# Kernel optimization log

Hardware: AMD Instinct MI355X
Metric: run time of the kernel (lower is better)

Reference implementation:

```python
import jax, jax.numpy as jnp
import numpy as np

TOP_K = 2


def setup_inputs() -> dict:
    key = jax.random.key(0)
    ks = jax.random.split(key, 5)
    B, N, C, FF, E = 2, 2048, 1024, 4096, 8
    x = jax.random.normal(ks[0], (B, N, C), dtype=jnp.float32)
    router_w = jax.random.normal(ks[1], (E, C), dtype=jnp.float32) * 0.02
    # xavier-uniform-like init for expert weights
    lim1 = np.sqrt(6.0 / (FF + C))
    expert_w1 = jax.random.uniform(ks[2], (E, FF, C), dtype=jnp.float32, minval=-lim1, maxval=lim1)
    expert_b1 = jnp.zeros((E, FF), dtype=jnp.float32)
    expert_w2 = jax.random.uniform(ks[3], (E, C, FF), dtype=jnp.float32, minval=-lim1, maxval=lim1)
    expert_b2 = jnp.zeros((E, C), dtype=jnp.float32)
    return {"x": x, "router_w": router_w, "expert_w1": expert_w1,
            "expert_b1": expert_b1, "expert_w2": expert_w2, "expert_b2": expert_b2}


def reference(x, router_w, expert_w1, expert_b1, expert_w2, expert_b2):
    # x: [B,N,C]; router_w: [E,C]; expert_w1: [E,FF,C]; expert_w2: [E,C,FF]
    router_logits = jnp.einsum('bnc,ec->bne', x, router_w)          # [B,N,E]
    router_probs = jax.nn.softmax(router_logits, axis=-1)
    expert_weights, expert_idx = jax.lax.top_k(router_probs, TOP_K)  # [B,N,K]
    expert_weights = expert_weights / (expert_weights.sum(axis=-1, keepdims=True) + 1e-9)
    # Dense all-expert FFN (avoids materializing per-token gathered weight matrices)
    h = jnp.einsum('bnc,efc->bnef', x, expert_w1) + expert_b1        # [B,N,E,FF]
    h = jax.nn.gelu(h, approximate=False)                            # torch nn.GELU = exact
    out_all = jnp.einsum('bnef,ecf->bnec', h, expert_w2) + expert_b2  # [B,N,E,C]
    # Gather top-k expert outputs and combine
    out_k = jnp.take_along_axis(out_all, expert_idx[..., None], axis=2)  # [B,N,K,C]
    return (out_k * expert_weights[..., None]).sum(axis=2)           # [B,N,C]
```

## Files before the change

kernel.cpp:

```cpp
#include <hip/hip_runtime.h>
#include <hip/hip_bf16.h>
#include <cstdint>

#define TTOK  4096
#define CDIM  1024
#define FFDIM 4096
#define NEXP  8


typedef short short8 __attribute__((ext_vector_type(8)));
typedef float f32x4 __attribute__((ext_vector_type(4)));

__device__ __forceinline__ unsigned short f2bf(float f) {
    unsigned int u = __float_as_uint(f);
    u = u + 0x7fffu + ((u >> 16) & 1u);
    return (unsigned short)(u >> 16);
}

__device__ __forceinline__ void gl_lds16(const unsigned short* g, unsigned short* l) {
    __builtin_amdgcn_global_load_lds(
        (const __attribute__((address_space(1))) unsigned int*)g,
        (__attribute__((address_space(3))) unsigned int*)l, 16, 0, 0);
}

__global__ void cast_kernel(const float* __restrict__ src, unsigned short* __restrict__ dst) {
    int i = blockIdx.x * blockDim.x + threadIdx.x;
    float4 v = reinterpret_cast<const float4*>(src)[i];
    ushort4 o;
    o.x = f2bf(v.x); o.y = f2bf(v.y); o.z = f2bf(v.z); o.w = f2bf(v.w);
    reinterpret_cast<ushort4*>(dst)[i] = o;
}

__global__ void router_kernel(const float* __restrict__ x, const float* __restrict__ rw,
                              int* __restrict__ counts, int* __restrict__ btok,
                              float* __restrict__ bgate) {
    const int wave = threadIdx.x >> 6;
    const int lane = threadIdx.x & 63;
    const int t = blockIdx.x * 4 + wave;
    const float* xr = x + (size_t)t * CDIM;

    float acc[NEXP];
#pragma unroll
    for (int e = 0; e < NEXP; e++) acc[e] = 0.f;
    for (int c = lane; c < CDIM; c += 64) {
        float xv = xr[c];
#pragma unroll
        for (int e = 0; e < NEXP; e++) acc[e] += xv * rw[e * CDIM + c];
    }
#pragma unroll
    for (int e = 0; e < NEXP; e++) {
#pragma unroll
        for (int off = 32; off > 0; off >>= 1) acc[e] += __shfl_down(acc[e], off, 64);
    }
    if (lane == 0) {
        float mx = acc[0];
#pragma unroll
        for (int e = 1; e < NEXP; e++) mx = fmaxf(mx, acc[e]);
        float p[NEXP]; float s = 0.f;
#pragma unroll
        for (int e = 0; e < NEXP; e++) { p[e] = expf(acc[e] - mx); s += p[e]; }
        int i0 = 0;
#pragma unroll
        for (int e = 1; e < NEXP; e++) if (p[e] > p[i0]) i0 = e;
        int i1 = (i0 == 0) ? 1 : 0;
#pragma unroll
        for (int e = 0; e < NEXP; e++) if (e != i0 && p[e] > p[i1]) i1 = e;
        float pr0 = p[i0] / s, pr1 = p[i1] / s;
        float rs = 1.f / (pr0 + pr1 + 1e-9f);
        float w0 = pr0 * rs, w1 = pr1 * rs;
        int pos = atomicAdd(&counts[i0], 1);
        btok[i0 * TTOK + pos] = t; bgate[i0 * TTOK + pos] = w0;
        pos = atomicAdd(&counts[i1], 1);
        btok[i1 * TTOK + pos] = t; bgate[i1 * TTOK + pos] = w1;
    }
}

__global__ void offsets_kernel(const int* __restrict__ counts, int* __restrict__ offsets) {
    if (threadIdx.x == 0 && blockIdx.x == 0) {
        int s = 0;
        for (int e = 0; e < NEXP; e++) { offsets[e] = s; s += counts[e]; }
        offsets[NEXP] = s;
    }
}


__global__ __launch_bounds__(256) void gemm1f_kernel(
    const unsigned short* __restrict__ xb, const unsigned short* __restrict__ w1b,
    const float* __restrict__ b1, const int* __restrict__ counts,
    const int* __restrict__ offsets, const int* __restrict__ btok,
    unsigned short* __restrict__ H) {
    const int e = blockIdx.z;
    const int cnt = counts[e];
    const int m0 = blockIdx.y * 128;
    if (m0 >= cnt) return;
    const int n0 = blockIdx.x * 128;
    const int po = offsets[e];

    __shared__ unsigned short As[128 * 32];
    __shared__ unsigned short Bs[128 * 32];
    __shared__ unsigned short Cs[64 * 128];

    const int tid = threadIdx.x;
    const int wave = tid >> 6, lane = tid & 63;
    const int wm = (wave >> 1) << 6, wn = (wave & 1) << 6;
    const int lm = lane & 15, kq = lane >> 4;

    const int sr = tid >> 2;
    const int sc = (tid & 3) << 3;
    const int tA0 = btok[e * TTOK + min(m0 + sr, cnt - 1)];
    const int tA1 = btok[e * TTOK + min(m0 + 64 + sr, cnt - 1)];
    const unsigned short* ga0 = xb + (size_t)tA0 * CDIM + sc;
    const unsigned short* ga1 = xb + (size_t)tA1 * CDIM + sc;
    const unsigned short* gb0 = w1b + ((size_t)e * FFDIM + n0 + sr) * CDIM + sc;
    const unsigned short* gb1 = gb0 + (size_t)64 * CDIM;
    unsigned short* lA = &As[tid * 8];
    unsigned short* lB = &Bs[tid * 8];

    f32x4 acc[4][4];
#pragma unroll
    for (int i = 0; i < 4; i++)
#pragma unroll
        for (int j = 0; j < 4; j++) { f32x4 z = {0.f, 0.f, 0.f, 0.f}; acc[i][j] = z; }

    for (int k0 = 0; k0 < CDIM; k0 += 32) {
        gl_lds16(ga0 + k0, lA);
        gl_lds16(ga1 + k0, lA + 64 * 32);
        gl_lds16(gb0 + k0, lB);
        gl_lds16(gb1 + k0, lB + 64 * 32);
        __syncthreads();
        short8 af[4], bfr[4];
#pragma unroll
        for (int i = 0; i < 4; i++) af[i] = *reinterpret_cast<const short8*>(&As[(wm + i * 16 + lm) * 32 + kq * 8]);
#pragma unroll
        for (int j = 0; j < 4; j++) bfr[j] = *reinterpret_cast<const short8*>(&Bs[(wn + j * 16 + lm) * 32 + kq * 8]);
#pragma unroll
        for (int i = 0; i < 4; i++)
#pragma unroll
            for (int j = 0; j < 4; j++)
                acc[i][j] = __builtin_amdgcn_mfma_f32_16x16x32_bf16(af[i], bfr[j], acc[i][j], 0, 0, 0);
        __syncthreads();
    }

    float bias[4];
#pragma unroll
    for (int j = 0; j < 4; j++) bias[j] = b1[e * FFDIM + n0 + wn + j * 16 + lm];

#pragma unroll
    for (int p = 0; p < 2; p++) {
        if ((wave >> 1) == p) {
#pragma unroll
            for (int i = 0; i < 4; i++) {
#pragma unroll
                for (int r = 0; r < 4; r++) {
                    const int row = i * 16 + kq * 4 + r;
#pragma unroll
                    for (int j = 0; j < 4; j++) {
                        float h = acc[i][j][r] + bias[j];
                        float g = 0.5f * h * (1.f + erff(h * 0.70710678118654752f));
                        Cs[row * 128 + wn + j * 16 + lm] = f2bf(g);
                    }
                }
            }
        }
        __syncthreads();
#pragma unroll
        for (int q = 0; q < 4; q++) {
            const int c = q * 256 + tid;
            const int row = c >> 4;
            const int col8 = (c & 15) << 3;
            const int mrow = m0 + p * 64 + row;
            if (mrow < cnt)
                *reinterpret_cast<uint4*>(&H[(size_t)(po + mrow) * FFDIM + n0 + col8]) =
                    *reinterpret_cast<const uint4*>(&Cs[row * 128 + col8]);
        }
        __syncthreads();
    }
}

__global__ __launch_bounds__(256) void gemm2f_kernel(
    const unsigned short* __restrict__ H, const unsigned short* __restrict__ w2b,
    const float* __restrict__ b2, const int* __restrict__ counts,
    const int* __restrict__ offsets, const int* __restrict__ btok,
    const float* __restrict__ bgate, float* __restrict__ out) {
    const int e = blockIdx.z;
    const int cnt = counts[e];
    const int m0 = (blockIdx.y >> 1) * 128;
    const int ks = blockIdx.y & 1;
    if (m0 >= cnt) return;
    const int n0 = blockIdx.x * 128;
    const int po = offsets[e];

    __shared__ unsigned short As[128 * 32];
    __shared__ unsigned short Bs[128 * 32];

    const int tid = threadIdx.x;
    const int wave = tid >> 6, lane = tid & 63;
    const int wm = (wave >> 1) << 6, wn = (wave & 1) << 6;
    const int lm = lane & 15, kq = lane >> 4;

    const int sr = tid >> 2;
    const int sc = (tid & 3) << 3;
    const int r0 = min(m0 + sr, cnt - 1);
    const int r1 = min(m0 + 64 + sr, cnt - 1);
    const unsigned short* ga0 = H + (size_t)(po + r0) * FFDIM + ks * 2048 + sc;
    const unsigned short* ga1 = H + (size_t)(po + r1) * FFDIM + ks * 2048 + sc;
    const unsigned short* gb0 = w2b + ((size_t)e * CDIM + n0 + sr) * FFDIM + ks * 2048 + sc;
    const unsigned short* gb1 = gb0 + (size_t)64 * FFDIM;
    unsigned short* lA = &As[tid * 8];
    unsigned short* lB = &Bs[tid * 8];

    f32x4 acc[4][4];
#pragma unroll
    for (int i = 0; i < 4; i++)
#pragma unroll
        for (int j = 0; j < 4; j++) { f32x4 z = {0.f, 0.f, 0.f, 0.f}; acc[i][j] = z; }

    for (int k0 = 0; k0 < 2048; k0 += 32) {
        gl_lds16(ga0 + k0, lA);
        gl_lds16(ga1 + k0, lA + 64 * 32);
        gl_lds16(gb0 + k0, lB);
        gl_lds16(gb1 + k0, lB + 64 * 32);
        __syncthreads();
        short8 af[4], bfr[4];
#pragma unroll
        for (int i = 0; i < 4; i++) af[i] = *reinterpret_cast<const short8*>(&As[(wm + i * 16 + lm) * 32 + kq * 8]);
#pragma unroll
        for (int j = 0; j < 4; j++) bfr[j] = *reinterpret_cast<const short8*>(&Bs[(wn + j * 16 + lm) * 32 + kq * 8]);
#pragma unroll
        for (int i = 0; i < 4; i++)
#pragma unroll
            for (int j = 0; j < 4; j++)
                acc[i][j] = __builtin_amdgcn_mfma_f32_16x16x32_bf16(af[i], bfr[j], acc[i][j], 0, 0, 0);
        __syncthreads();
    }

    float bias[4];
#pragma unroll
    for (int j = 0; j < 4; j++) bias[j] = (ks == 0) ? b2[e * CDIM + n0 + wn + j * 16 + lm] : 0.f;

#pragma unroll
    for (int i = 0; i < 4; i++) {
#pragma unroll
        for (int r = 0; r < 4; r++) {
            const int mrow = m0 + wm + i * 16 + kq * 4 + r;
            if (mrow < cnt) {
                const int tok = btok[e * TTOK + mrow];
                const float g = bgate[e * TTOK + mrow];
                float* orow = out + (size_t)tok * CDIM;
#pragma unroll
                for (int j = 0; j < 4; j++)
                    atomicAdd(orow + n0 + wn + j * 16 + lm, g * (acc[i][j][r] + bias[j]));
            }
        }
    }
}


__global__ __launch_bounds__(256) void gemm1_kernel(
    const unsigned short* __restrict__ xb, const float* __restrict__ w1,
    const float* __restrict__ b1, const int* __restrict__ counts,
    const int* __restrict__ offsets, const int* __restrict__ btok,
    unsigned short* __restrict__ H) {
    const int e = blockIdx.z;
    const int cnt = counts[e];
    const int m0 = blockIdx.y * 128;
    if (m0 >= cnt) return;
    const int n0 = blockIdx.x * 128;
    const int po = offsets[e];

    __shared__ unsigned short As[128][32];
    __shared__ unsigned short Bs[128][32];

    const int tid = threadIdx.x;
    const int wave = tid >> 6, lane = tid & 63;
    const int wm = (wave >> 1) << 6, wn = (wave & 1) << 6;
    const int lm = lane & 15, kq = lane >> 4;

    f32x4 acc[4][4];
#pragma unroll
    for (int i = 0; i < 4; i++)
#pragma unroll
        for (int j = 0; j < 4; j++) { f32x4 z = {0.f, 0.f, 0.f, 0.f}; acc[i][j] = z; }

    const float* w1e = w1 + (size_t)e * FFDIM * CDIM;
    const int arow = tid >> 1;
    const int acolb = (tid & 1) * 16;
    int tokA = -1;
    if (m0 + arow < cnt) tokA = btok[e * TTOK + m0 + arow];
    const int brow = tid >> 1;
    const int bcol = (tid & 1) * 16;

    for (int k0 = 0; k0 < CDIM; k0 += 32) {
        uint4 a0 = {0, 0, 0, 0}, a1 = {0, 0, 0, 0};
        if (tokA >= 0) {
            const uint4* src = reinterpret_cast<const uint4*>(xb + (size_t)tokA * CDIM + k0 + acolb);
            a0 = src[0]; a1 = src[1];
        }
        *reinterpret_cast<uint4*>(&As[arow][acolb]) = a0;
        *reinterpret_cast<uint4*>(&As[arow][acolb + 8]) = a1;
        {
            const float* src = w1e + (size_t)(n0 + brow) * CDIM + k0 + bcol;
            ushort4* dst = reinterpret_cast<ushort4*>(&Bs[brow][bcol]);
#pragma unroll
            for (int q = 0; q < 4; q++) {
                float4 v = reinterpret_cast<const float4*>(src)[q];
                ushort4 o; o.x = f2bf(v.x); o.y = f2bf(v.y); o.z = f2bf(v.z); o.w = f2bf(v.w);
                dst[q] = o;
            }
        }
        __syncthreads();
        short8 af[4], bfr[4];
#pragma unroll
        for (int i = 0; i < 4; i++) af[i] = *reinterpret_cast<const short8*>(&As[wm + i * 16 + lm][kq * 8]);
#pragma unroll
        for (int j = 0; j < 4; j++) bfr[j] = *reinterpret_cast<const short8*>(&Bs[wn + j * 16 + lm][kq * 8]);
#pragma unroll
        for (int i = 0; i < 4; i++)
#pragma unroll
            for (int j = 0; j < 4; j++)
                acc[i][j] = __builtin_amdgcn_mfma_f32_16x16x32_bf16(af[i], bfr[j], acc[i][j], 0, 0, 0);
        __syncthreads();
    }

#pragma unroll
    for (int j = 0; j < 4; j++) {
        const int fcol = n0 + wn + j * 16 + lm;
        const float bias = b1[e * FFDIM + fcol];
#pragma unroll
        for (int i = 0; i < 4; i++) {
#pragma unroll
            for (int r = 0; r < 4; r++) {
                const int mrow = m0 + wm + i * 16 + kq * 4 + r;
                if (mrow < cnt) {
                    float h = acc[i][j][r] + bias;
                    float g = 0.5f * h * (1.f + erff(h * 0.70710678118654752f));
                    H[(size_t)(po + mrow) * FFDIM + fcol] = f2bf(g);
                }
            }
        }
    }
}

__global__ __launch_bounds__(256) void gemm2_kernel(
    const unsigned short* __restrict__ H, const float* __restrict__ w2,
    const float* __restrict__ b2, const int* __restrict__ counts,
    const int* __restrict__ offsets, const int* __restrict__ btok,
    const float* __restrict__ bgate, float* __restrict__ out) {
    const int e = blockIdx.z;
    const int cnt = counts[e];
    const int m0 = blockIdx.y * 128;
    if (m0 >= cnt) return;
    const int n0 = blockIdx.x * 128;
    const int po = offsets[e];

    __shared__ unsigned short As[128][32];
    __shared__ unsigned short Bs[128][32];

    const int tid = threadIdx.x;
    const int wave = tid >> 6, lane = tid & 63;
    const int wm = (wave >> 1) << 6, wn = (wave & 1) << 6;
    const int lm = lane & 15, kq = lane >> 4;

    f32x4 acc[4][4];
#pragma unroll
    for (int i = 0; i < 4; i++)
#pragma unroll
        for (int j = 0; j < 4; j++) { f32x4 z = {0.f, 0.f, 0.f, 0.f}; acc[i][j] = z; }

    const float* w2e = w2 + (size_t)e * CDIM * FFDIM;
    const int arow = tid >> 1;
    const int acolb = (tid & 1) * 16;
    const bool aval = (m0 + arow < cnt);
    const unsigned short* asrc = H + (size_t)(po + m0 + arow) * FFDIM + acolb;
    const int brow = tid >> 1;
    const int bcol = (tid & 1) * 16;

    for (int k0 = 0; k0 < FFDIM; k0 += 32) {
        uint4 a0 = {0, 0, 0, 0}, a1 = {0, 0, 0, 0};
        if (aval) {
            const uint4* src = reinterpret_cast<const uint4*>(asrc + k0);
            a0 = src[0]; a1 = src[1];
        }
        *reinterpret_cast<uint4*>(&As[arow][acolb]) = a0;
        *reinterpret_cast<uint4*>(&As[arow][acolb + 8]) = a1;
        {
            const float* src = w2e + (size_t)(n0 + brow) * FFDIM + k0 + bcol;
            ushort4* dst = reinterpret_cast<ushort4*>(&Bs[brow][bcol]);
#pragma unroll
            for (int q = 0; q < 4; q++) {
                float4 v = reinterpret_cast<const float4*>(src)[q];
                ushort4 o; o.x = f2bf(v.x); o.y = f2bf(v.y); o.z = f2bf(v.z); o.w = f2bf(v.w);
                dst[q] = o;
            }
        }
        __syncthreads();
        short8 af[4], bfr[4];
#pragma unroll
        for (int i = 0; i < 4; i++) af[i] = *reinterpret_cast<const short8*>(&As[wm + i * 16 + lm][kq * 8]);
#pragma unroll
        for (int j = 0; j < 4; j++) bfr[j] = *reinterpret_cast<const short8*>(&Bs[wn + j * 16 + lm][kq * 8]);
#pragma unroll
        for (int i = 0; i < 4; i++)
#pragma unroll
            for (int j = 0; j < 4; j++)
                acc[i][j] = __builtin_amdgcn_mfma_f32_16x16x32_bf16(af[i], bfr[j], acc[i][j], 0, 0, 0);
        __syncthreads();
    }

    float bias[4];
#pragma unroll
    for (int j = 0; j < 4; j++) bias[j] = b2[e * CDIM + n0 + wn + j * 16 + lm];

#pragma unroll
    for (int i = 0; i < 4; i++) {
#pragma unroll
        for (int r = 0; r < 4; r++) {
            const int mrow = m0 + wm + i * 16 + kq * 4 + r;
            if (mrow < cnt) {
                const int tok = btok[e * TTOK + mrow];
                const float g = bgate[e * TTOK + mrow];
                float* orow = out + (size_t)tok * CDIM;
#pragma unroll
                for (int j = 0; j < 4; j++) {
                    const int c = n0 + wn + j * 16 + lm;
                    atomicAdd(orow + c, g * (acc[i][j][r] + bias[j]));
                }
            }
        }
    }
}

extern "C" void kernel_launch(void* const* d_in, const int* in_sizes, int n_in,
                              void* d_out, int out_size, void* d_ws, size_t ws_size,
                              hipStream_t stream) {
    const float* x  = (const float*)d_in[0];
    const float* rw = (const float*)d_in[1];
    const float* w1 = (const float*)d_in[2];
    const float* b1 = (const float*)d_in[3];
    const float* w2 = (const float*)d_in[4];
    const float* b2 = (const float*)d_in[5];
    float* out = (float*)d_out;

    char* ws = (char*)d_ws;
    int*   counts  = (int*)ws;
    int*   offsets = (int*)(ws + 64);
    int*   btok    = (int*)(ws + 4096);
    float* bgate   = (float*)(ws + 4096 + 131072);

    hipMemsetAsync(d_out, 0, (size_t)out_size * sizeof(float), stream);
    hipMemsetAsync(counts, 0, 64, stream);

    const bool fast = ws_size >= ((size_t)137 << 20);

    if (fast) {
        unsigned short* xb = (unsigned short*)(ws + ((size_t)1 << 20));
        unsigned short* Wb = (unsigned short*)(ws + ((size_t)9 << 20));
        unsigned short* H  = (unsigned short*)(ws + ((size_t)73 << 20));

        cast_kernel<<<(TTOK * CDIM) / (256 * 4), 256, 0, stream>>>(x, xb);
        router_kernel<<<TTOK / 4, 256, 0, stream>>>(x, rw, counts, btok, bgate);
        offsets_kernel<<<1, 64, 0, stream>>>(counts, offsets);
        cast_kernel<<<(NEXP * FFDIM * CDIM) / (256 * 4), 256, 0, stream>>>(w1, Wb);
        gemm1f_kernel<<<dim3(FFDIM / 128, TTOK / 128, NEXP), 256, 0, stream>>>(
            xb, Wb, b1, counts, offsets, btok, H);
        cast_kernel<<<(NEXP * CDIM * FFDIM) / (256 * 4), 256, 0, stream>>>(w2, Wb);
        gemm2f_kernel<<<dim3(CDIM / 128, (TTOK / 128) * 2, NEXP), 256, 0, stream>>>(
            H, Wb, b2, counts, offsets, btok, bgate, out);
    } else {
        unsigned short* xb = (unsigned short*)(ws + ((size_t)1 << 20));
        unsigned short* H  = (unsigned short*)(ws + ((size_t)16 << 20));

        cast_kernel<<<(TTOK * CDIM) / (256 * 4), 256, 0, stream>>>(x, xb);
        router_kernel<<<TTOK / 4, 256, 0, stream>>>(x, rw, counts, btok, bgate);
        offsets_kernel<<<1, 64, 0, stream>>>(counts, offsets);
        gemm1_kernel<<<dim3(FFDIM / 128, TTOK / 128, NEXP), 256, 0, stream>>>(
            xb, w1, b1, counts, offsets, btok, H);
        gemm2_kernel<<<dim3(CDIM / 128, TTOK / 128, NEXP), 256, 0, stream>>>(
            H, w2, b2, counts, offsets, btok, bgate, out);
    }
}
```

Before: 708.4 us.

## Double-buffer LDS tiles in both expert GEMM kernels with one barrier per step

Both expert GEMM kernels now stage A/B tiles in a two-slot shared buffer. The next K-slice is issued via global_load_lds into the idle slot while MFMAs consume the current one. This drops the trailing barrier in each K step and aims to hide global load latency behind compute. The risk is that the compiler inserts conservative vmcnt waits before the LDS reads, which would serialize the loads again. The epilogue staging buffer in gemm1 now aliases the tile memory, so shared usage is unchanged.

Measured after the change: 691.4 us. -2.4%, faster.

```diff
diff --git a/kernel.cpp b/kernel.cpp
--- a/kernel.cpp
+++ b/kernel.cpp
@@ -96,9 +96,8 @@
     const int n0 = blockIdx.x * 128;
     const int po = offsets[e];
 
-    __shared__ unsigned short As[128 * 32];
-    __shared__ unsigned short Bs[128 * 32];
-    __shared__ unsigned short Cs[64 * 128];
+    __shared__ uint4 smem4[2048];
+    unsigned short* smem = (unsigned short*)smem4;
 
     const int tid = threadIdx.x;
     const int wave = tid >> 6, lane = tid & 63;
@@ -113,8 +112,6 @@
     const unsigned short* ga1 = xb + (size_t)tA1 * CDIM + sc;
     const unsigned short* gb0 = w1b + ((size_t)e * FFDIM + n0 + sr) * CDIM + sc;
     const unsigned short* gb1 = gb0 + (size_t)64 * CDIM;
-    unsigned short* lA = &As[tid * 8];
-    unsigned short* lB = &Bs[tid * 8];
 
     f32x4 acc[4][4];
 #pragma unroll
@@ -122,12 +119,26 @@
 #pragma unroll
         for (int j = 0; j < 4; j++) { f32x4 z = {0.f, 0.f, 0.f, 0.f}; acc[i][j] = z; }
 
+    {
+        unsigned short* base = smem;
+        gl_lds16(ga0, base + tid * 8);
+        gl_lds16(ga1, base + 64 * 32 + tid * 8);
+        gl_lds16(gb0, base + 4096 + tid * 8);
+        gl_lds16(gb1, base + 4096 + 64 * 32 + tid * 8);
+    }
+
     for (int k0 = 0; k0 < CDIM; k0 += 32) {
-        gl_lds16(ga0 + k0, lA);
-        gl_lds16(ga1 + k0, lA + 64 * 32);
-        gl_lds16(gb0 + k0, lB);
-        gl_lds16(gb1 + k0, lB + 64 * 32);
-        __syncthreads();
+        const int cur = (k0 >> 5) & 1;
+        __syncthreads();
+        if (k0 + 32 < CDIM) {
+            unsigned short* base = smem + (cur ^ 1) * 8192;
+            gl_lds16(ga0 + k0 + 32, base + tid * 8);
+            gl_lds16(ga1 + k0 + 32, base + 64 * 32 + tid * 8);
+            gl_lds16(gb0 + k0 + 32, base + 4096 + tid * 8);
+            gl_lds16(gb1 + k0 + 32, base + 4096 + 64 * 32 + tid * 8);
+        }
+        const unsigned short* As = smem + cur * 8192;
+        const unsigned short* Bs = As + 4096;
         short8 af[4], bfr[4];
 #pragma unroll
         for (int i = 0; i < 4; i++) af[i] = *reinterpret_cast<const short8*>(&As[(wm + i * 16 + lm) * 32 + kq * 8]);
@@ -138,13 +149,14 @@
 #pragma unroll
             for (int j = 0; j < 4; j++)
                 acc[i][j] = __builtin_amdgcn_mfma_f32_16x16x32_bf16(af[i], bfr[j], acc[i][j], 0, 0, 0);
-        __syncthreads();
-    }
+    }
+    __syncthreads();
 
     float bias[4];
 #pragma unroll
     for (int j = 0; j < 4; j++) bias[j] = b1[e * FFDIM + n0 + wn + j * 16 + lm];
 
+    unsigned short* Cs = smem;
 #pragma unroll
     for (int p = 0; p < 2; p++) {
         if ((wave >> 1) == p) {
@@ -190,8 +202,8 @@
     const int n0 = blockIdx.x * 128;
     const int po = offsets[e];
 
-    __shared__ unsigned short As[128 * 32];
-    __shared__ unsigned short Bs[128 * 32];
+    __shared__ uint4 smem4[2048];
+    unsigned short* smem = (unsigned short*)smem4;
 
     const int tid = threadIdx.x;
     const int wave = tid >> 6, lane = tid & 63;
@@ -206,8 +218,6 @@
     const unsigned short* ga1 = H + (size_t)(po + r1) * FFDIM + ks * 2048 + sc;
     const unsigned short* gb0 = w2b + ((size_t)e * CDIM + n0 + sr) * FFDIM + ks * 2048 + sc;
     const unsigned short* gb1 = gb0 + (size_t)64 * FFDIM;
-    unsigned short* lA = &As[tid * 8];
-    unsigned short* lB = &Bs[tid * 8];
 
     f32x4 acc[4][4];
 #pragma unroll
@@ -215,12 +225,26 @@
 #pragma unroll
         for (int j = 0; j < 4; j++) { f32x4 z = {0.f, 0.f, 0.f, 0.f}; acc[i][j] = z; }
 
+    {
+        unsigned short* base = smem;
+        gl_lds16(ga0, base + tid * 8);
+        gl_lds16(ga1, base + 64 * 32 + tid * 8);
+        gl_lds16(gb0, base + 4096 + tid * 8);
+        gl_lds16(gb1, base + 4096 + 64 * 32 + tid * 8);
+    }
+
     for (int k0 = 0; k0 < 2048; k0 += 32) {
-        gl_lds16(ga0 + k0, lA);
-        gl_lds16(ga1 + k0, lA + 64 * 32);
-        gl_lds16(gb0 + k0, lB);
-        gl_lds16(gb1 + k0, lB + 64 * 32);
-        __syncthreads();
+        const int cur = (k0 >> 5) & 1;
+        __syncthreads();
+        if (k0 + 32 < 2048) {
+            unsigned short* base = smem + (cur ^ 1) * 8192;
+            gl_lds16(ga0 + k0 + 32, base + tid * 8);
+            gl_lds16(ga1 + k0 + 32, base + 64 * 32 + tid * 8);
+            gl_lds16(gb0 + k0 + 32, base + 4096 + tid * 8);
+            gl_lds16(gb1 + k0 + 32, base + 4096 + 64 * 32 + tid * 8);
+        }
+        const unsigned short* As = smem + cur * 8192;
+        const unsigned short* Bs = As + 4096;
         short8 af[4], bfr[4];
 #pragma unroll
         for (int i = 0; i < 4; i++) af[i] = *reinterpret_cast<const short8*>(&As[(wm + i * 16 + lm) * 32 + kq * 8]);
@@ -231,7 +255,6 @@
 #pragma unroll
             for (int j = 0; j < 4; j++)
                 acc[i][j] = __builtin_amdgcn_mfma_f32_16x16x32_bf16(af[i], bfr[j], acc[i][j], 0, 0, 0);
-        __syncthreads();
     }
 
     float bias[4];
```

## Double-buffer LDS with register-staged prefetch in both expert GEMMs

Applied to the files above, without the earlier changes.

Replaces the direct global-to-LDS loads, which needed two barriers per k-step and left no overlap, with a software pipeline in both grouped GEMMs. Tiles are prefetched into registers two steps ahead and written into alternating LDS buffers, so global latency overlaps MFMA work and there is one barrier per k-step. The cost is more VGPRs for the staged tiles, which may lower occupancy, and extra VALU/LDS store instructions in place of the direct-to-LDS path. The LDS region is also reused as the GELU output staging buffer in gemm1.

After: 1.327 ms. 87.3% more time.

```diff
diff --git a/kernel.cpp b/kernel.cpp
--- a/kernel.cpp
+++ b/kernel.cpp
@@ -15,12 +15,6 @@
     unsigned int u = __float_as_uint(f);
     u = u + 0x7fffu + ((u >> 16) & 1u);
     return (unsigned short)(u >> 16);
-}
-
-__device__ __forceinline__ void gl_lds16(const unsigned short* g, unsigned short* l) {
-    __builtin_amdgcn_global_load_lds(
-        (const __attribute__((address_space(1))) unsigned int*)g,
-        (__attribute__((address_space(3))) unsigned int*)l, 16, 0, 0);
 }
 
 __global__ void cast_kernel(const float* __restrict__ src, unsigned short* __restrict__ dst) {
@@ -83,6 +77,33 @@
     }
 }
 
+
+#define GLOAD(s, kk) do { \
+    ra0[s] = *reinterpret_cast<const uint4*>(ga0 + (kk)); \
+    ra1[s] = *reinterpret_cast<const uint4*>(ga1 + (kk)); \
+    rb0[s] = *reinterpret_cast<const uint4*>(gb0 + (kk)); \
+    rb1[s] = *reinterpret_cast<const uint4*>(gb1 + (kk)); } while (0)
+
+#define SWRITE(s) do { \
+    unsigned short* base_ = smem + (s) * 8192; \
+    *reinterpret_cast<uint4*>(base_ + tid * 8)        = ra0[s]; \
+    *reinterpret_cast<uint4*>(base_ + 2048 + tid * 8) = ra1[s]; \
+    *reinterpret_cast<uint4*>(base_ + 4096 + tid * 8) = rb0[s]; \
+    *reinterpret_cast<uint4*>(base_ + 6144 + tid * 8) = rb1[s]; } while (0)
+
+#define COMPUTE(buf) do { \
+    const unsigned short* As_ = smem + (buf) * 8192; \
+    const unsigned short* Bs_ = As_ + 4096; \
+    short8 af[4], bfr[4]; \
+    _Pragma("unroll") \
+    for (int i = 0; i < 4; i++) af[i] = *reinterpret_cast<const short8*>(&As_[(wm + i * 16 + lm) * 32 + kq * 8]); \
+    _Pragma("unroll") \
+    for (int j = 0; j < 4; j++) bfr[j] = *reinterpret_cast<const short8*>(&Bs_[(wn + j * 16 + lm) * 32 + kq * 8]); \
+    _Pragma("unroll") \
+    for (int i = 0; i < 4; i++) \
+        _Pragma("unroll") \
+        for (int j = 0; j < 4; j++) \
+            acc[i][j] = __builtin_amdgcn_mfma_f32_16x16x32_bf16(af[i], bfr[j], acc[i][j], 0, 0, 0); } while (0)
 
 __global__ __launch_bounds__(256) void gemm1f_kernel(
     const unsigned short* __restrict__ xb, const unsigned short* __restrict__ w1b,
@@ -96,9 +117,8 @@
     const int n0 = blockIdx.x * 128;
     const int po = offsets[e];
 
-    __shared__ unsigned short As[128 * 32];
-    __shared__ unsigned short Bs[128 * 32];
-    __shared__ unsigned short Cs[64 * 128];
+    __shared__ uint4 smem4[2048];
+    unsigned short* smem = (unsigned short*)smem4;
 
     const int tid = threadIdx.x;
     const int wave = tid >> 6, lane = tid & 63;
@@ -113,8 +133,6 @@
     const unsigned short* ga1 = xb + (size_t)tA1 * CDIM + sc;
     const unsigned short* gb0 = w1b + ((size_t)e * FFDIM + n0 + sr) * CDIM + sc;
     const unsigned short* gb1 = gb0 + (size_t)64 * CDIM;
-    unsigned short* lA = &As[tid * 8];
-    unsigned short* lB = &Bs[tid * 8];
 
     f32x4 acc[4][4];
 #pragma unroll
@@ -122,29 +140,30 @@
 #pragma unroll
         for (int j = 0; j < 4; j++) { f32x4 z = {0.f, 0.f, 0.f, 0.f}; acc[i][j] = z; }
 
-    for (int k0 = 0; k0 < CDIM; k0 += 32) {
-        gl_lds16(ga0 + k0, lA);
-        gl_lds16(ga1 + k0, lA + 64 * 32);
-        gl_lds16(gb0 + k0, lB);
-        gl_lds16(gb1 + k0, lB + 64 * 32);
-        __syncthreads();
-        short8 af[4], bfr[4];
-#pragma unroll
-        for (int i = 0; i < 4; i++) af[i] = *reinterpret_cast<const short8*>(&As[(wm + i * 16 + lm) * 32 + kq * 8]);
-#pragma unroll
-        for (int j = 0; j < 4; j++) bfr[j] = *reinterpret_cast<const short8*>(&Bs[(wn + j * 16 + lm) * 32 + kq * 8]);
-#pragma unroll
-        for (int i = 0; i < 4; i++)
-#pragma unroll
-            for (int j = 0; j < 4; j++)
-                acc[i][j] = __builtin_amdgcn_mfma_f32_16x16x32_bf16(af[i], bfr[j], acc[i][j], 0, 0, 0);
-        __syncthreads();
-    }
+    uint4 ra0[2], ra1[2], rb0[2], rb1[2];
+    const int KT = CDIM / 32;
+
+    GLOAD(0, 0);
+    GLOAD(1, 32);
+    SWRITE(0);
+    __syncthreads();
+
+    for (int k = 0; k < KT; k += 2) {
+        if (k + 2 < KT) GLOAD(0, (k + 2) * 32);
+        COMPUTE(0);
+        SWRITE(1);
+        __syncthreads();
+        if (k + 3 < KT) GLOAD(1, (k + 3) * 32);
+        COMPUTE(1);
+        if (k + 2 < KT) { SWRITE(0); __syncthreads(); }
+    }
+    __syncthreads();
 
     float bias[4];
 #pragma unroll
     for (int j = 0; j < 4; j++) bias[j] = b1[e * FFDIM + n0 + wn + j * 16 + lm];
 
+    unsigned short* Cs = smem;
 #pragma unroll
     for (int p = 0; p < 2; p++) {
         if ((wave >> 1) == p) {
@@ -190,8 +209,8 @@
     const int n0 = blockIdx.x * 128;
     const int po = offsets[e];
 
-    __shared__ unsigned short As[128 * 32];
-    __shared__ unsigned short Bs[128 * 32];
+    __shared__ uint4 smem4[2048];
+    unsigned short* smem = (unsigned short*)smem4;
 
     const int tid = threadIdx.x;
     const int wave = tid >> 6, lane = tid & 63;
@@ -206,8 +225,6 @@
     const unsigned short* ga1 = H + (size_t)(po + r1) * FFDIM + ks * 2048 + sc;
     const unsigned short* gb0 = w2b + ((size_t)e * CDIM + n0 + sr) * FFDIM + ks * 2048 + sc;
     const unsigned short* gb1 = gb0 + (size_t)64 * FFDIM;
-    unsigned short* lA = &As[tid * 8];
-    unsigned short* lB = &Bs[tid * 8];
 
     f32x4 acc[4][4];
 #pragma unroll
@@ -215,23 +232,22 @@
 #pragma unroll
         for (int j = 0; j < 4; j++) { f32x4 z = {0.f, 0.f, 0.f, 0.f}; acc[i][j] = z; }
 
-    for (int k0 = 0; k0 < 2048; k0 += 32) {
-        gl_lds16(ga0 + k0, lA);
-        gl_lds16(ga1 + k0, lA + 64 * 32);
-        gl_lds16(gb0 + k0, lB);
-        gl_lds16(gb1 + k0, lB + 64 * 32);
-        __syncthreads();
-        short8 af[4], bfr[4];
-#pragma unroll
-        for (int i = 0; i < 4; i++) af[i] = *reinterpret_cast<const short8*>(&As[(wm + i * 16 + lm) * 32 + kq * 8]);
-#pragma unroll
-        for (int j = 0; j < 4; j++) bfr[j] = *reinterpret_cast<const short8*>(&Bs[(wn + j * 16 + lm) * 32 + kq * 8]);
-#pragma unroll
-        for (int i = 0; i < 4; i++)
-#pragma unroll
-            for (int j = 0; j < 4; j++)
-                acc[i][j] = __builtin_amdgcn_mfma_f32_16x16x32_bf16(af[i], bfr[j], acc[i][j], 0, 0, 0);
-        __syncthreads();
+    uint4 ra0[2], ra1[2], rb0[2], rb1[2];
+    const int KT = 2048 / 32;
+
+    GLOAD(0, 0);
+    GLOAD(1, 32);
+    SWRITE(0);
+    __syncthreads();
+
+    for (int k = 0; k < KT; k += 2) {
+        if (k + 2 < KT) GLOAD(0, (k + 2) * 32);
+        COMPUTE(0);
+        SWRITE(1);
+        __syncthreads();
+        if (k + 3 < KT) GLOAD(1, (k + 3) * 32);
+        COMPUTE(1);
+        if (k + 2 < KT) { SWRITE(0); __syncthreads(); }
     }
 
     float bias[4];
```
